# Optimization experiments

Measured on AMD Instinct MI355X. Metric: run time of the kernel, lower is better.

The kernel has to match this reference:

```python
import jax, jax.numpy as jnp
import numpy as np

N_CELLS, D_IN, D_HID, D_OUT, MLP_W = 16384, 512, 1024, 512, 128
N_FACTIONS, SYNC, DEBATE = 8, 0.15, 0.15


def setup_inputs() -> dict:
    key = jax.random.key(0)
    ks = jax.random.split(key, 20)
    s = 0.05
    inp = {
        "x": jax.random.normal(ks[0], (1, D_IN), jnp.float32),
        "hiddens": jax.random.normal(ks[1], (N_CELLS, D_HID), jnp.float32) * 0.1,
        "wealth_norm": jax.random.uniform(ks[2], (N_CELLS,), jnp.float32, 0.5, 1.5),
        "Wa1": jax.random.normal(ks[3], (D_IN + D_HID, MLP_W), jnp.float32) * s,
        "ba1": jax.random.normal(ks[4], (MLP_W,), jnp.float32) * s,
        "Wa2": jax.random.normal(ks[5], (MLP_W, D_OUT), jnp.float32) * s,
        "ba2": jax.random.normal(ks[6], (D_OUT,), jnp.float32) * s,
        "Wg1": jax.random.normal(ks[7], (D_IN + D_HID, MLP_W), jnp.float32) * s,
        "bg1": jax.random.normal(ks[8], (MLP_W,), jnp.float32) * s,
        "Wg2": jax.random.normal(ks[9], (MLP_W, D_OUT), jnp.float32) * s,
        "bg2": jax.random.normal(ks[10], (D_OUT,), jnp.float32) * s,
        "W_ih": jax.random.normal(ks[11], (D_OUT + 1, 3 * D_HID), jnp.float32) * s,
        "W_hh": jax.random.normal(ks[12], (D_HID, 3 * D_HID), jnp.float32) * s,
        "b_ih": jax.random.normal(ks[13], (3 * D_HID,), jnp.float32) * s,
        "b_hh": jax.random.normal(ks[14], (3 * D_HID,), jnp.float32) * s,
        "Wo": jax.random.normal(ks[15], (D_OUT, D_IN), jnp.float32) * s,
        "bo": jax.random.normal(ks[16], (D_IN,), jnp.float32) * s,
        "positions": jax.random.randint(ks[17], (N_CELLS,), 0, 3, jnp.int32) - 1,
        "step": 10,
    }
    return inp


def _gru_cell(mem, h, W_ih, W_hh, b_ih, b_hh):
    # torch.nn.GRUCell math, gate order r, z, n
    gi = mem @ W_ih + b_ih            # [N, 3H]
    gh = h @ W_hh + b_hh              # [N, 3H]
    gi_r, gi_z, gi_n = jnp.split(gi, 3, axis=-1)
    gh_r, gh_z, gh_n = jnp.split(gh, 3, axis=-1)
    r = jax.nn.sigmoid(gi_r + gh_r)
    z = jax.nn.sigmoid(gi_z + gh_z)
    n = jnp.tanh(gi_n + r * gh_n)
    return (1.0 - z) * n + z * h


def _group_sync(h, mask):
    cnt = jnp.sum(mask)
    m = mask[:, None].astype(h.dtype)
    mean = jnp.sum(h * m, axis=0) / jnp.maximum(cnt, 1).astype(h.dtype)
    blended = 0.9 * h + 0.1 * mean
    return jnp.where((mask[:, None]) & (cnt >= 2), blended, h)


def _faction_sync_debate(h, step):
    n = h.shape[0]
    n_f = min(N_FACTIONS, n // 2)
    if n_f < 2:
        return h
    fs = n // n_f
    hf = h[: n_f * fs].reshape(n_f, fs, -1)
    fmean = hf.mean(axis=1, keepdims=True)                    # [n_f, 1, H]
    hf = (1.0 - SYNC) * hf + SYNC * fmean
    if step > 5:
        global_op = hf.mean(axis=1).mean(axis=0)              # [H]
        dc = max(1, fs // 4)
        head = (1.0 - DEBATE) * hf[:, :dc] + DEBATE * global_op
        hf = jnp.concatenate([head, hf[:, dc:]], axis=1)
    out = hf.reshape(n_f * fs, -1)
    if n_f * fs < n:
        out = jnp.concatenate([out, h[n_f * fs:]], axis=0)
    return out


def reference(x, hiddens, wealth_norm, Wa1, ba1, Wa2, ba2, Wg1, bg1, Wg2, bg2,
              W_ih, W_hh, b_ih, b_hh, Wo, bo, positions, step):
    n = hiddens.shape[0]
    xb = jnp.broadcast_to(x, (n, x.shape[-1]))                # same x for every cell
    combined = jnp.concatenate([xb, hiddens], axis=-1)        # [N, D_in+D_hid]
    a = jax.nn.relu(combined @ Wa1 + ba1) @ Wa2 + ba2
    g = jax.nn.relu(combined @ Wg1 + bg1) @ Wg2 + bg2
    output = a - g                                            # [N, D_out]
    tension = jnp.mean(output ** 2, axis=-1, keepdims=True)   # [N, 1]
    mem_input = jax.lax.stop_gradient(jnp.concatenate([output, tension], axis=-1))
    new_h = _gru_cell(mem_input, hiddens, W_ih, W_hh, b_ih, b_hh)
    mod = 0.9 + 0.1 * jnp.clip(wealth_norm, 0.1, 2.0)
    new_h = jnp.clip(new_h * mod[:, None], -10.0, 10.0)
    new_h = jax.lax.stop_gradient(new_h)                      # original detaches state
    new_h = _group_sync(new_h, positions > 0)
    new_h = _group_sync(new_h, positions < 0)
    new_h = _faction_sync_debate(new_h, step)
    # tension weights come from .item() in torch -> constants
    weights = jax.nn.softmax(jax.lax.stop_gradient(tension[:, 0]))
    combined_out = weights @ output                           # [D_out]
    pred = (combined_out @ Wo + bo)[None, :]                  # [1, D_in]
    avg_tension = jnp.mean(tension)
    return pred, avg_tension, new_h
```

## Files before the change

kernel.cpp:

```cpp
#include <hip/hip_runtime.h>
#include <stdint.h>

typedef unsigned short u16;
typedef __bf16 bf16x8 __attribute__((ext_vector_type(8)));
typedef float f32x4 __attribute__((ext_vector_type(4)));


__device__ __forceinline__ float bf2f(unsigned u) { return __uint_as_float(u << 16); }
__device__ __forceinline__ u16 f2bf(float f) {
  unsigned x = __float_as_uint(f);
  unsigned r = x + 0x7fffu + ((x >> 16) & 1u);
  return (u16)(r >> 16);
}
__device__ __forceinline__ unsigned pack2(float a, float b) {
  return (unsigned)f2bf(a) | ((unsigned)f2bf(b) << 16);
}
__device__ __forceinline__ float sigm(float x) { return 1.f / (1.f + __expf(-x)); }
__device__ __forceinline__ float fast_tanh(float x) {
  float e = __expf(2.f * x);
  return 1.f - 2.f / (e + 1.f);
}

#define AS1(p) ((const __attribute__((address_space(1))) void*)(p))
#define AS3(p) ((__attribute__((address_space(3))) void*)(p))

#define NC 16384

__device__ __forceinline__ void packT_body(
    const float* __restrict__ src, int sld, int srow0,
    u16* __restrict__ dst, int dld, int drow0, int koff,
    int remapThresh, int remapAdd, float sgn, int bx, int by,
    float (*tile)[65], int t) {
  const int k0 = by * 64, c0 = bx * 64;
  const int tx = t & 15, ty = t >> 4;
#pragma unroll
  for (int p = 0; p < 4; ++p) {
    int r = ty + p * 16;
    float4 v = *reinterpret_cast<const float4*>(&src[(size_t)(srow0 + k0 + r) * sld + c0 + tx * 4]);
    tile[tx * 4 + 0][r] = v.x;
    tile[tx * 4 + 1][r] = v.y;
    tile[tx * 4 + 2][r] = v.z;
    tile[tx * 4 + 3][r] = v.w;
  }
  __syncthreads();
  const int cl = t >> 2;
  const int kb = (t & 3) * 16;
  int col = c0 + cl;
  int row = drow0 + col + ((col >= remapThresh) ? remapAdd : 0);
  union { u16 o[16]; uint4 v[2]; } u;
#pragma unroll
  for (int e = 0; e < 16; ++e) u.o[e] = f2bf(sgn * tile[cl][kb + e]);
  uint4* d = reinterpret_cast<uint4*>(&dst[(size_t)row * dld + koff + k0 + kb]);
  d[0] = u.v[0]; d[1] = u.v[1];
}

__global__ __launch_bounds__(256) void prep_kernel(
    const float* __restrict__ hid, u16* __restrict__ hidc,
    const float* __restrict__ W_ih, const float* __restrict__ W_hh, u16* __restrict__ WgruT,
    const float* __restrict__ Wa1, const float* __restrict__ Wg1, u16* __restrict__ W1catT,
    const float* __restrict__ Wa2, const float* __restrict__ Wg2, u16* __restrict__ W2catT,
    const float* __restrict__ x, const float* __restrict__ ba1, const float* __restrict__ bg1,
    float* __restrict__ bias1, const float* __restrict__ ba2, const float* __restrict__ bg2,
    float* __restrict__ bias2, const int* __restrict__ positions, int* __restrict__ counts) {
  __shared__ float tile[64][65];
  int b = blockIdx.x, t = threadIdx.x;
  if (b < 16384) {
    int i = b * 256 + t;
    float4 v = ((const float4*)hid)[i];
    uint2 o; o.x = pack2(v.x, v.y); o.y = pack2(v.z, v.w);
    ((uint2*)hidc)[i] = o;
    return;
  }
  b -= 16384;
  if (b < 768) {
    packT_body(W_hh, 3072, 0, WgruT, 1536, 0, 512, 2048, 1024, 1.f, b % 48, b / 48, tile, t);
    return;
  }
  b -= 768;
  if (b < 384) {
    packT_body(W_ih, 3072, 0, WgruT, 1536, 0, 0, 1 << 30, 0, 1.f, b % 48, b / 48, tile, t);
    return;
  }
  b -= 384;
  if (b < 32) { packT_body(Wa1, 128, 512, W1catT, 1024, 0, 0, 1 << 30, 0, 1.f, b % 2, b / 2, tile, t); return; }
  b -= 32;
  if (b < 32) { packT_body(Wg1, 128, 512, W1catT, 1024, 128, 0, 1 << 30, 0, 1.f, b % 2, b / 2, tile, t); return; }
  b -= 32;
  if (b < 16) { packT_body(Wa2, 512, 0, W2catT, 256, 0, 0, 1 << 30, 0, 1.f, b % 8, b / 8, tile, t); return; }
  b -= 16;
  if (b < 16) { packT_body(Wg2, 512, 0, W2catT, 256, 0, 128, 1 << 30, 0, -1.f, b % 8, b / 8, tile, t); return; }
  b -= 16;
  if (b < 8) {
    const float* W = (t < 128) ? Wa1 : Wg1;
    int cc = t & 127;
    float acc = 0.f;
    int k0 = b * 64;
    for (int k = k0; k < k0 + 64; ++k) acc += x[k] * W[(size_t)k * 128 + cc];
    if (b == 0) acc += (t < 128) ? ba1[cc] : bg1[cc];
    atomicAdd(&bias1[t], acc);
    return;
  }
  b -= 8;
  if (b < 2) { int n = b * 256 + t; bias2[n] = ba2[n] - bg2[n]; return; }
  b -= 2;
  {
    int i = b * 256 + t;
    int p = positions[i], f = i >> 11;
    if (p > 0) atomicAdd(&counts[f * 2], 1);
    else if (p < 0) atomicAdd(&counts[f * 2 + 1], 1);
  }
}

__global__ __launch_bounds__(256) void gemm_bt(
    const u16* __restrict__ A, int lda,
    const u16* __restrict__ Bt, int ldb,
    u16* __restrict__ C, int ldc,
    const float* __restrict__ bias, int epi, int K,
    float* __restrict__ tension) {
  __shared__ __align__(16) u16 As[128 * 32];
  __shared__ __align__(16) u16 Bs[128 * 32];
  const int tid = threadIdx.x;
  const int m0 = blockIdx.x * 128;
  const int n0 = blockIdx.y * 128;
  f32x4 acc[4][4] = {};
  const int lane = tid & 63;
  const int w = tid >> 6;
  const int mw = (w & 1) * 64, nw = (w >> 1) * 64;
  const int fr = lane & 15;
  const int q = lane >> 4;
  const int ar0 = tid >> 2;
  const int ag = ((tid & 3) ^ ((ar0 >> 1) & 3)) * 8;

  for (int kk = 0; kk < K; kk += 32) {
    __syncthreads();
    __builtin_amdgcn_global_load_lds(AS1(A + (size_t)(m0 + ar0) * lda + kk + ag), AS3(&As[tid * 8]), 16, 0, 0);
    __builtin_amdgcn_global_load_lds(AS1(A + (size_t)(m0 + ar0 + 64) * lda + kk + ag), AS3(&As[(tid + 256) * 8]), 16, 0, 0);
    __builtin_amdgcn_global_load_lds(AS1(Bt + (size_t)(n0 + ar0) * ldb + kk + ag), AS3(&Bs[tid * 8]), 16, 0, 0);
    __builtin_amdgcn_global_load_lds(AS1(Bt + (size_t)(n0 + ar0 + 64) * ldb + kk + ag), AS3(&Bs[(tid + 256) * 8]), 16, 0, 0);
    __syncthreads();
    bf16x8 af[4], bfv[4];
#pragma unroll
    for (int mt = 0; mt < 4; ++mt) {
      int r = mw + mt * 16 + fr;
      af[mt] = *reinterpret_cast<const bf16x8*>(&As[r * 32 + ((q ^ ((r >> 1) & 3)) * 8)]);
    }
#pragma unroll
    for (int nt = 0; nt < 4; ++nt) {
      int r = nw + nt * 16 + fr;
      bfv[nt] = *reinterpret_cast<const bf16x8*>(&Bs[r * 32 + ((q ^ ((r >> 1) & 3)) * 8)]);
    }
#pragma unroll
    for (int mt = 0; mt < 4; ++mt)
#pragma unroll
      for (int nt = 0; nt < 4; ++nt)
        acc[mt][nt] = __builtin_amdgcn_mfma_f32_16x16x32_bf16(af[mt], bfv[nt], acc[mt][nt], 0, 0, 0);
  }
  const int rq = q * 4;
#pragma unroll
  for (int mt = 0; mt < 4; ++mt) {
    float srow[4] = {0.f, 0.f, 0.f, 0.f};
#pragma unroll
    for (int nt = 0; nt < 4; ++nt) {
      int col = n0 + nw + nt * 16 + fr;
      f32x4 v = acc[mt][nt];
#pragma unroll
      for (int r = 0; r < 4; ++r) {
        int row = m0 + mw + mt * 16 + rq + r;
        float val = v[r] + bias[col];
        if (epi == 1) val = val > 0.f ? val : 0.f;
        else srow[r] += val * val;
        C[(size_t)row * ldc + col] = f2bf(val);
      }
    }
    if (epi == 3) {
#pragma unroll
      for (int r = 0; r < 4; ++r) {
        float s = srow[r];
        s += __shfl_xor(s, 1, 16); s += __shfl_xor(s, 2, 16);
        s += __shfl_xor(s, 4, 16); s += __shfl_xor(s, 8, 16);
        if (fr == 0) atomicAdd(&tension[m0 + mw + mt * 16 + rq + r], s);
      }
    }
  }
}

__global__ __launch_bounds__(512, 4) void gemm_gru(
    const u16* __restrict__ outbf, const u16* __restrict__ hidc,
    const u16* __restrict__ WgruT,
    const float* __restrict__ W_ihf, const float* __restrict__ bihf,
    const float* __restrict__ bhhf, const float* __restrict__ wealthf,
    const float* __restrict__ tension, u16* __restrict__ hpre) {
  __shared__ __align__(16) u16 As[128 * 32];
  __shared__ __align__(16) u16 Bs[3][64 * 32];
  const int tid = threadIdx.x;
  const int m0 = blockIdx.x * 128;
  const int j0 = blockIdx.y * 64;
  f32x4 acc[4][2][2] = {};
  const int lane = tid & 63;
  const int w = tid >> 6;
  const int mw = (w & 3) * 32, nw = (w >> 2) * 32;
  const int fr = lane & 15;
  const int q = lane >> 4;
  const int arow = tid >> 2;
  const int ag = ((tid & 3) ^ ((arow >> 1) & 3)) * 8;
  const int ct = tid & 255;
  const int brow = ct >> 2;
  const int bg = ((ct & 3) ^ ((brow >> 1) & 3)) * 8;
  const int bsel = tid >> 8;

#pragma unroll
  for (int phase = 0; phase < 2; ++phase) {
    const u16* Ap = phase ? hidc : outbf;
    const int lda = phase ? 1024 : 512;
    const int kbeg = phase ? 512 : 0;
    const int kend = phase ? 1536 : 512;
    const int growG = phase ? 3072 : 2048;
#pragma unroll 1
    for (int kk = kbeg; kk < kend; kk += 32) {
      const int ka = kk - kbeg;
      __syncthreads();
      __builtin_amdgcn_global_load_lds(AS1(Ap + (size_t)(m0 + arow) * lda + ka + ag), AS3(&As[tid * 8]), 16, 0, 0);
      if (bsel == 0) {
        __builtin_amdgcn_global_load_lds(AS1(WgruT + (size_t)(j0 + brow) * 1536 + kk + bg), AS3(&Bs[0][ct * 8]), 16, 0, 0);
        __builtin_amdgcn_global_load_lds(AS1(WgruT + (size_t)(growG + j0 + brow) * 1536 + kk + bg), AS3(&Bs[2][ct * 8]), 16, 0, 0);
      } else {
        __builtin_amdgcn_global_load_lds(AS1(WgruT + (size_t)(1024 + j0 + brow) * 1536 + kk + bg), AS3(&Bs[1][ct * 8]), 16, 0, 0);
      }
      __syncthreads();
      bf16x8 af[2], b0[2], b1[2], b2[2];
#pragma unroll
      for (int mt = 0; mt < 2; ++mt) {
        int r = mw + mt * 16 + fr;
        af[mt] = *reinterpret_cast<const bf16x8*>(&As[r * 32 + ((q ^ ((r >> 1) & 3)) * 8)]);
      }
#pragma unroll
      for (int nt = 0; nt < 2; ++nt) {
        int r = nw + nt * 16 + fr;
        int s = (q ^ ((r >> 1) & 3)) * 8;
        b0[nt] = *reinterpret_cast<const bf16x8*>(&Bs[0][r * 32 + s]);
        b1[nt] = *reinterpret_cast<const bf16x8*>(&Bs[1][r * 32 + s]);
        b2[nt] = *reinterpret_cast<const bf16x8*>(&Bs[2][r * 32 + s]);
      }
#pragma unroll
      for (int mt = 0; mt < 2; ++mt)
#pragma unroll
        for (int nt = 0; nt < 2; ++nt) {
          acc[0][mt][nt] = __builtin_amdgcn_mfma_f32_16x16x32_bf16(af[mt], b0[nt], acc[0][mt][nt], 0, 0, 0);
          acc[1][mt][nt] = __builtin_amdgcn_mfma_f32_16x16x32_bf16(af[mt], b1[nt], acc[1][mt][nt], 0, 0, 0);
          if (phase == 0)
            acc[2][mt][nt] = __builtin_amdgcn_mfma_f32_16x16x32_bf16(af[mt], b2[nt], acc[2][mt][nt], 0, 0, 0);
          else
            acc[3][mt][nt] = __builtin_amdgcn_mfma_f32_16x16x32_bf16(af[mt], b2[nt], acc[3][mt][nt], 0, 0, 0);
        }
    }
  }

  const int rq = q * 4;
  const float* wt = W_ihf + (size_t)512 * 3072;
  float wtr[2], wtz[2], wtn[2], bir[2], biz[2], bin_[2], bhr_[2], bhz_[2], bhn_[2];
#pragma unroll
  for (int nt = 0; nt < 2; ++nt) {
    int j = j0 + nw + nt * 16 + fr;
    wtr[nt] = wt[j]; wtz[nt] = wt[1024 + j]; wtn[nt] = wt[2048 + j];
    bir[nt] = bihf[j]; biz[nt] = bihf[1024 + j]; bin_[nt] = bihf[2048 + j];
    bhr_[nt] = bhhf[j]; bhz_[nt] = bhhf[1024 + j]; bhn_[nt] = bhhf[2048 + j];
  }
#pragma unroll
  for (int mt = 0; mt < 2; ++mt) {
#pragma unroll
    for (int rr = 0; rr < 4; ++rr) {
      int row = m0 + mw + mt * 16 + rq + rr;
      float tv = tension[row] * (1.f / 512.f);
      float wl = fminf(fmaxf(wealthf[row], 0.1f), 2.0f);
      float mod = 0.9f + 0.1f * wl;
#pragma unroll
      for (int nt = 0; nt < 2; ++nt) {
        int j = j0 + nw + nt * 16 + fr;
        float r = sigm(acc[0][mt][nt][rr] + tv * wtr[nt] + bir[nt] + bhr_[nt]);
        float z = sigm(acc[1][mt][nt][rr] + tv * wtz[nt] + biz[nt] + bhz_[nt]);
        float n = fast_tanh(acc[2][mt][nt][rr] + tv * wtn[nt] + bin_[nt]
                            + r * (acc[3][mt][nt][rr] + bhn_[nt]));
        float h = bf2f(hidc[(size_t)row * 1024 + j]);
        float h2 = (1.f - z) * n + z * h;
        h2 = fminf(fmaxf(h2 * mod, -10.f), 10.f);
        hpre[(size_t)row * 1024 + j] = f2bf(h2);
      }
    }
  }
}

__global__ void stats_kernel(const u16* __restrict__ hpre, const int* __restrict__ positions,
                             float* __restrict__ fsums) {
  int cc = blockIdx.x, f = blockIdx.y, z = blockIdx.z, t = threadIdx.x;
  int col = cc * 128 + (t & 127);
  int half = t >> 7;
  float st = 0, sp = 0, sm = 0;
  for (int it = 0; it < 128; ++it) {
    int row = (f << 11) + ((z * 128 + it) << 1) + half;
    int p = positions[row];
    float v = bf2f(hpre[(size_t)row * 1024 + col]);
    st += v;
    if (p > 0) sp += v;
    if (p < 0) sm += v;
  }
  atomicAdd(&fsums[(f * 3 + 0) * 1024 + col], st);
  atomicAdd(&fsums[(f * 3 + 1) * 1024 + col], sp);
  atomicAdd(&fsums[(f * 3 + 2) * 1024 + col], sm);
}

__global__ void derive_kernel(const float* __restrict__ fsums, const int* __restrict__ counts,
                              float* __restrict__ mean1, float* __restrict__ mean2,
                              float* __restrict__ fmean, float* __restrict__ gop,
                              float* __restrict__ scal) {
  int c = threadIdx.x;
  int cnt1 = 0, cnt2 = 0, cf1[8], cf2[8];
#pragma unroll
  for (int f = 0; f < 8; ++f) {
    cf1[f] = counts[f * 2]; cf2[f] = counts[f * 2 + 1];
    cnt1 += cf1[f]; cnt2 += cf2[f];
  }
  float s1 = 0, s2 = 0;
#pragma unroll
  for (int f = 0; f < 8; ++f) { s1 += fsums[(f * 3 + 1) * 1024 + c]; s2 += fsums[(f * 3 + 2) * 1024 + c]; }
  float m1 = s1 / (float)(cnt1 > 1 ? cnt1 : 1);
  float m2 = s2 / (float)(cnt2 > 1 ? cnt2 : 1);
  float a1 = (cnt1 >= 2) ? 0.1f : 0.f;
  float a2 = (cnt2 >= 2) ? 0.1f : 0.f;
  float g = 0;
#pragma unroll
  for (int f = 0; f < 8; ++f) {
    float fm = (fsums[(f * 3) * 1024 + c]
                + a1 * ((float)cf1[f] * m1 - fsums[(f * 3 + 1) * 1024 + c])
                + a2 * ((float)cf2[f] * m2 - fsums[(f * 3 + 2) * 1024 + c])) * (1.f / 2048.f);
    fmean[f * 1024 + c] = fm;
    g += fm;
  }
  gop[c] = g * 0.125f;
  mean1[c] = m1; mean2[c] = m2;
  if (c == 0) { scal[0] = a1; scal[1] = a2; }
}

__global__ void finalize_kernel(const u16* __restrict__ hpre, const int* __restrict__ positions,
                                const int* __restrict__ step, const float* __restrict__ mean1,
                                const float* __restrict__ mean2, const float* __restrict__ fmean,
                                const float* __restrict__ gop, const float* __restrict__ scal,
                                float* __restrict__ out) {
  int row = blockIdx.x, t = threadIdx.x;
  int p = positions[row];
  float w1 = (p > 0) ? scal[0] : 0.f;
  float w2 = (p < 0) ? scal[1] : 0.f;
  int f = row >> 11, q = row & 2047;
  bool deb = (step[0] > 5) && (q < 512);
  const u16* hrow = hpre + (size_t)row * 1024;
  const float* fmp = fmean + f * 1024;
  float* orow = out + 513 + (size_t)row * 1024;
#pragma unroll
  for (int e = 0; e < 8; ++e) {
    int c = e * 128 + t;
    float h = bf2f(hrow[c]);
    float hgs = h + w1 * (mean1[c] - h) + w2 * (mean2[c] - h);
    float hfs = 0.85f * hgs + 0.15f * fmp[c];
    orow[c] = deb ? (0.85f * hfs + 0.15f * gop[c]) : hfs;
  }
}

__global__ void softmax_kernel(const float* __restrict__ tension, float* __restrict__ weights,
                               float* __restrict__ out) {
  __shared__ float red[1024];
  int t = threadIdx.x;
  float tv[16], mx = -1e30f, sumt = 0.f;
#pragma unroll
  for (int k = 0; k < 16; ++k) {
    tv[k] = tension[t + k * 1024] * (1.f / 512.f);
    mx = fmaxf(mx, tv[k]); sumt += tv[k];
  }
  red[t] = mx; __syncthreads();
  for (int s = 512; s > 0; s >>= 1) { if (t < s) red[t] = fmaxf(red[t], red[t + s]); __syncthreads(); }
  float m = red[0]; __syncthreads();
  red[t] = sumt; __syncthreads();
  for (int s = 512; s > 0; s >>= 1) { if (t < s) red[t] += red[t + s]; __syncthreads(); }
  float tot = red[0]; __syncthreads();
  float ev[16], se = 0.f;
#pragma unroll
  for (int k = 0; k < 16; ++k) { ev[k] = __expf(tv[k] - m); se += ev[k]; }
  red[t] = se; __syncthreads();
  for (int s = 512; s > 0; s >>= 1) { if (t < s) red[t] += red[t + s]; __syncthreads(); }
  float invS = 1.f / red[0];
#pragma unroll
  for (int k = 0; k < 16; ++k) weights[t + k * 1024] = ev[k] * invS;
  if (t == 0) out[512] = tot * (1.f / 16384.f);
}

__global__ void wsum_kernel(const float* __restrict__ weights, const u16* __restrict__ outbf,
                            float* __restrict__ co) {
  int b = blockIdx.x, t = threadIdx.x;
  int c = t * 2;
  float a0 = 0.f, a1 = 0.f;
  int i0 = b * 128;
  for (int i = i0; i < i0 + 128; ++i) {
    float w = weights[i];
    unsigned v = *reinterpret_cast<const unsigned*>(outbf + (size_t)i * 512 + c);
    a0 += w * bf2f(v & 0xffff);
    a1 += w * bf2f(v >> 16);
  }
  atomicAdd(&co[c], a0);
  atomicAdd(&co[c + 1], a1);
}

__global__ void pred_kernel(const float* __restrict__ co, const float* __restrict__ Wof,
                            const float* __restrict__ bof, float* __restrict__ out) {
  __shared__ float cs[512];
  int t = threadIdx.x, n = blockIdx.x * 256 + t;
  cs[t] = co[t]; cs[t + 256] = co[t + 256];
  __syncthreads();
  float acc = bof[n];
  for (int ck = 0; ck < 512; ++ck) acc += cs[ck] * Wof[(size_t)ck * 512 + n];
  out[n] = acc;
}

extern "C" void kernel_launch(void* const* d_in, const int* in_sizes, int n_in,
                              void* d_out, int out_size, void* d_ws, size_t ws_size,
                              hipStream_t stream) {
  const float* x      = (const float*)d_in[0];
  const float* hid    = (const float*)d_in[1];
  const float* wealth = (const float*)d_in[2];
  const float* Wa1    = (const float*)d_in[3];
  const float* ba1    = (const float*)d_in[4];
  const float* Wa2    = (const float*)d_in[5];
  const float* ba2    = (const float*)d_in[6];
  const float* Wg1    = (const float*)d_in[7];
  const float* bg1    = (const float*)d_in[8];
  const float* Wg2    = (const float*)d_in[9];
  const float* bg2    = (const float*)d_in[10];
  const float* W_ih   = (const float*)d_in[11];
  const float* W_hh   = (const float*)d_in[12];
  const float* b_ih   = (const float*)d_in[13];
  const float* b_hh   = (const float*)d_in[14];
  const float* Wo     = (const float*)d_in[15];
  const float* bo     = (const float*)d_in[16];
  const int* positions= (const int*)d_in[17];
  const int* step     = (const int*)d_in[18];
  float* out = (float*)d_out;

  char* w = (char*)d_ws;
  size_t off = 0;
  auto alloc = [&](size_t bytes) { void* p = w + off; off += (bytes + 255) & ~(size_t)255; return p; };
  u16*   hidc    = (u16*)  alloc((size_t)NC * 1024 * 2);
  u16*   outbf   = (u16*)  alloc((size_t)NC * 512 * 2);
  u16*   hpre    = (u16*)  alloc((size_t)NC * 1024 * 2);
  u16*   WgruT   = (u16*)  alloc((size_t)4096 * 1536 * 2);
  u16*   W1catT  = (u16*)  alloc((size_t)256 * 1024 * 2);
  u16*   W2catT  = (u16*)  alloc((size_t)512 * 256 * 2);
  u16*   t1      = (u16*)  alloc((size_t)NC * 256 * 2);
  float* bias1   = (float*)alloc(256 * 4);
  float* co      = (float*)alloc(512 * 4);
  int*   counts  = (int*)  alloc(16 * 4);
  float* fsums   = (float*)alloc(8 * 3 * 1024 * 4);
  float* tension = (float*)alloc(NC * 4);
  float* bias2   = (float*)alloc(512 * 4);
  float* weights = (float*)alloc(NC * 4);
  float* mean1   = (float*)alloc(1024 * 4);
  float* mean2   = (float*)alloc(1024 * 4);
  float* gop     = (float*)alloc(1024 * 4);
  float* fmean   = (float*)alloc(8 * 1024 * 4);
  float* scal    = (float*)alloc(8 * 4);

  hipMemsetAsync(bias1, 0, 1024 + 2048 + 256 + 98304 + 65536, stream);

  prep_kernel<<<17706, 256, 0, stream>>>(hid, hidc, W_ih, W_hh, WgruT,
                                         Wa1, Wg1, W1catT, Wa2, Wg2, W2catT,
                                         x, ba1, bg1, bias1, ba2, bg2, bias2,
                                         positions, counts);

  gemm_bt<<<dim3(128, 2), 256, 0, stream>>>(hidc, 1024, W1catT, 1024, t1, 256,
                                            bias1, 1, 1024, nullptr);
  gemm_bt<<<dim3(128, 4), 256, 0, stream>>>(t1, 256, W2catT, 256, outbf, 512,
                                            bias2, 3, 256, tension);

  gemm_gru<<<dim3(128, 16), 512, 0, stream>>>(outbf, hidc, WgruT, W_ih, b_ih, b_hh,
                                              wealth, tension, hpre);

  stats_kernel<<<dim3(8, 8, 8), 256, 0, stream>>>(hpre, positions, fsums);
  derive_kernel<<<1, 1024, 0, stream>>>(fsums, counts, mean1, mean2, fmean, gop, scal);
  finalize_kernel<<<NC, 128, 0, stream>>>(hpre, positions, step, mean1, mean2, fmean, gop,
                                          scal, out);

  softmax_kernel<<<1, 1024, 0, stream>>>(tension, weights, out);
  wsum_kernel<<<128, 256, 0, stream>>>(weights, outbf, co);
  pred_kernel<<<2, 256, 0, stream>>>(co, Wo, bo, out);

  (void)in_sizes; (void)n_in; (void)out_size; (void)ws_size;
}
```

Baseline: 602.7 us.

## Triple-buffer LDS tiles with async prefetch in GEMM and GRU kernels

Both the generic bf16 GEMM and the fused GRU GEMM now keep three LDS stages and issue global_load_lds prefetches two k-steps ahead. Explicit vmcnt waits replace the two __syncthreads per iteration, and the MFMA block runs under raised wave priority. This is meant to hide global-memory latency behind the matrix math. The cost is triple the LDS footprint, which may reduce occupancy (especially for gemm_gru with 512-thread blocks and launch bounds 4). The hand-counted waitcnt values also add correctness risk.

```diff
diff --git a/kernel.cpp b/kernel.cpp
--- a/kernel.cpp
+++ b/kernel.cpp
@@ -117,8 +117,8 @@
     u16* __restrict__ C, int ldc,
     const float* __restrict__ bias, int epi, int K,
     float* __restrict__ tension) {
-  __shared__ __align__(16) u16 As[128 * 32];
-  __shared__ __align__(16) u16 Bs[128 * 32];
+  __shared__ __align__(16) u16 As[3][128 * 32];
+  __shared__ __align__(16) u16 Bs[3][128 * 32];
   const int tid = threadIdx.x;
   const int m0 = blockIdx.x * 128;
   const int n0 = blockIdx.y * 128;
@@ -131,29 +131,52 @@
   const int ar0 = tid >> 2;
   const int ag = ((tid & 3) ^ ((ar0 >> 1) & 3)) * 8;
 
-  for (int kk = 0; kk < K; kk += 32) {
-    __syncthreads();
-    __builtin_amdgcn_global_load_lds(AS1(A + (size_t)(m0 + ar0) * lda + kk + ag), AS3(&As[tid * 8]), 16, 0, 0);
-    __builtin_amdgcn_global_load_lds(AS1(A + (size_t)(m0 + ar0 + 64) * lda + kk + ag), AS3(&As[(tid + 256) * 8]), 16, 0, 0);
-    __builtin_amdgcn_global_load_lds(AS1(Bt + (size_t)(n0 + ar0) * ldb + kk + ag), AS3(&Bs[tid * 8]), 16, 0, 0);
-    __builtin_amdgcn_global_load_lds(AS1(Bt + (size_t)(n0 + ar0 + 64) * ldb + kk + ag), AS3(&Bs[(tid + 256) * 8]), 16, 0, 0);
-    __syncthreads();
+  const u16* aB0 = A + (size_t)(m0 + ar0) * lda + ag;
+  const u16* aB1 = A + (size_t)(m0 + ar0 + 64) * lda + ag;
+  const u16* bB0 = Bt + (size_t)(n0 + ar0) * ldb + ag;
+  const u16* bB1 = Bt + (size_t)(n0 + ar0 + 64) * ldb + ag;
+
+  auto stage = [&](int kk, int buf) {
+    __builtin_amdgcn_global_load_lds(AS1(aB0 + kk), AS3(&As[buf][tid * 8]), 16, 0, 0);
+    __builtin_amdgcn_global_load_lds(AS1(aB1 + kk), AS3(&As[buf][(tid + 256) * 8]), 16, 0, 0);
+    __builtin_amdgcn_global_load_lds(AS1(bB0 + kk), AS3(&Bs[buf][tid * 8]), 16, 0, 0);
+    __builtin_amdgcn_global_load_lds(AS1(bB1 + kk), AS3(&Bs[buf][(tid + 256) * 8]), 16, 0, 0);
+  };
+
+  const int NT = K >> 5;
+  stage(0, 0);
+  stage(32, 1);
+  int cur = 0, nxt = 1, nx2 = 2;
+#pragma unroll 1
+  for (int t = 0; t < NT; ++t) {
+    if (t + 2 < NT) stage((t + 2) * 32, nx2);
+    const int rem = NT - 1 - t;
+    if (rem >= 2)      asm volatile("s_waitcnt vmcnt(8)" ::: "memory");
+    else if (rem == 1) asm volatile("s_waitcnt vmcnt(4)" ::: "memory");
+    else               asm volatile("s_waitcnt vmcnt(0)" ::: "memory");
+    __builtin_amdgcn_s_barrier();
+    asm volatile("" ::: "memory");
     bf16x8 af[4], bfv[4];
 #pragma unroll
     for (int mt = 0; mt < 4; ++mt) {
       int r = mw + mt * 16 + fr;
-      af[mt] = *reinterpret_cast<const bf16x8*>(&As[r * 32 + ((q ^ ((r >> 1) & 3)) * 8)]);
+      af[mt] = *reinterpret_cast<const bf16x8*>(&As[cur][r * 32 + ((q ^ ((r >> 1) & 3)) * 8)]);
     }
 #pragma unroll
     for (int nt = 0; nt < 4; ++nt) {
       int r = nw + nt * 16 + fr;
-      bfv[nt] = *reinterpret_cast<const bf16x8*>(&Bs[r * 32 + ((q ^ ((r >> 1) & 3)) * 8)]);
+      bfv[nt] = *reinterpret_cast<const bf16x8*>(&Bs[cur][r * 32 + ((q ^ ((r >> 1) & 3)) * 8)]);
     }
+    __builtin_amdgcn_s_setprio(1);
 #pragma unroll
     for (int mt = 0; mt < 4; ++mt)
 #pragma unroll
       for (int nt = 0; nt < 4; ++nt)
         acc[mt][nt] = __builtin_amdgcn_mfma_f32_16x16x32_bf16(af[mt], bfv[nt], acc[mt][nt], 0, 0, 0);
+    __builtin_amdgcn_s_setprio(0);
+    asm volatile("s_waitcnt lgkmcnt(0)" ::: "memory");
+    __builtin_amdgcn_s_barrier();
+    int tmp = cur; cur = nxt; nxt = nx2; nx2 = tmp;
   }
   const int rq = q * 4;
 #pragma unroll
@@ -190,8 +213,8 @@
     const float* __restrict__ W_ihf, const float* __restrict__ bihf,
     const float* __restrict__ bhhf, const float* __restrict__ wealthf,
     const float* __restrict__ tension, u16* __restrict__ hpre) {
-  __shared__ __align__(16) u16 As[128 * 32];
-  __shared__ __align__(16) u16 Bs[3][64 * 32];
+  __shared__ __align__(16) u16 As[3][128 * 32];
+  __shared__ __align__(16) u16 Bs[3][3][64 * 32];
   const int tid = threadIdx.x;
   const int m0 = blockIdx.x * 128;
   const int j0 = blockIdx.y * 64;
@@ -208,52 +231,77 @@
   const int bg = ((ct & 3) ^ ((brow >> 1) & 3)) * 8;
   const int bsel = tid >> 8;
 
-#pragma unroll
-  for (int phase = 0; phase < 2; ++phase) {
-    const u16* Ap = phase ? hidc : outbf;
-    const int lda = phase ? 1024 : 512;
-    const int kbeg = phase ? 512 : 0;
-    const int kend = phase ? 1536 : 512;
-    const int growG = phase ? 3072 : 2048;
+  const u16* aB0 = outbf + (size_t)(m0 + arow) * 512 + ag;
+  const u16* aB1 = hidc + (size_t)(m0 + arow) * 1024 + ag;
+  const u16* bBR = WgruT + (size_t)((bsel ? 1024 : 0) + j0 + brow) * 1536 + bg;
+
+  auto stage = [&](int s, int buf) {
+    const int p = s >= 16;
+    const u16* ap = p ? (aB1 + (s - 16) * 32) : (aB0 + s * 32);
+    __builtin_amdgcn_global_load_lds(AS1(ap), AS3(&As[buf][tid * 8]), 16, 0, 0);
+    const int kk = s * 32;
+    if (bsel == 0) {
+      __builtin_amdgcn_global_load_lds(AS1(bBR + kk), AS3(&Bs[buf][0][ct * 8]), 16, 0, 0);
+      __builtin_amdgcn_global_load_lds(
+          AS1(bBR + (size_t)(2048 * 1536 + (p ? 1024 * 1536 : 0) + kk)),
+          AS3(&Bs[buf][2][ct * 8]), 16, 0, 0);
+    } else {
+      __builtin_amdgcn_global_load_lds(AS1(bBR + kk), AS3(&Bs[buf][1][ct * 8]), 16, 0, 0);
+    }
+  };
+
+  stage(0, 0);
+  stage(1, 1);
+  int cur = 0, nxt = 1, nx2 = 2;
+
+#define GRU_STEP(T, REG3)                                                                     \
+  {                                                                                           \
+    if ((T) < 46) {                                                                           \
+      stage((T) + 2, nx2);                                                                    \
+      if (bsel == 0) asm volatile("s_waitcnt vmcnt(6)" ::: "memory");                         \
+      else           asm volatile("s_waitcnt vmcnt(4)" ::: "memory");                         \
+    } else if ((T) == 46) {                                                                   \
+      if (bsel == 0) asm volatile("s_waitcnt vmcnt(3)" ::: "memory");                         \
+      else           asm volatile("s_waitcnt vmcnt(2)" ::: "memory");                         \
+    } else {                                                                                  \
+      asm volatile("s_waitcnt vmcnt(0)" ::: "memory");                                        \
+    }                                                                                         \
+    __builtin_amdgcn_s_barrier();                                                             \
+    asm volatile("" ::: "memory");                                                            \
+    bf16x8 af[2], b0v[2], b1v[2], b2v[2];                                                     \
+    _Pragma("unroll")                                                                         \
+    for (int mt = 0; mt < 2; ++mt) {                                                          \
+      int r = mw + mt * 16 + fr;                                                              \
+      af[mt] = *reinterpret_cast<const bf16x8*>(&As[cur][r * 32 + ((q ^ ((r >> 1) & 3)) * 8)]);\
+    }                                                                                         \
+    _Pragma("unroll")                                                                         \
+    for (int nt = 0; nt < 2; ++nt) {                                                          \
+      int r = nw + nt * 16 + fr;                                                              \
+      int ss = (q ^ ((r >> 1) & 3)) * 8;                                                      \
+      b0v[nt] = *reinterpret_cast<const bf16x8*>(&Bs[cur][0][r * 32 + ss]);                   \
+      b1v[nt] = *reinterpret_cast<const bf16x8*>(&Bs[cur][1][r * 32 + ss]);                   \
+      b2v[nt] = *reinterpret_cast<const bf16x8*>(&Bs[cur][2][r * 32 + ss]);                   \
+    }                                                                                         \
+    __builtin_amdgcn_s_setprio(1);                                                            \
+    _Pragma("unroll")                                                                         \
+    for (int mt = 0; mt < 2; ++mt)                                                            \
+      _Pragma("unroll")                                                                       \
+      for (int nt = 0; nt < 2; ++nt) {                                                        \
+        acc[0][mt][nt] = __builtin_amdgcn_mfma_f32_16x16x32_bf16(af[mt], b0v[nt], acc[0][mt][nt], 0, 0, 0); \
+        acc[1][mt][nt] = __builtin_amdgcn_mfma_f32_16x16x32_bf16(af[mt], b1v[nt], acc[1][mt][nt], 0, 0, 0); \
+        acc[REG3][mt][nt] = __builtin_amdgcn_mfma_f32_16x16x32_bf16(af[mt], b2v[nt], acc[REG3][mt][nt], 0, 0, 0); \
+      }                                                                                       \
+    __builtin_amdgcn_s_setprio(0);                                                            \
+    asm volatile("s_waitcnt lgkmcnt(0)" ::: "memory");                                        \
+    __builtin_amdgcn_s_barrier();                                                             \
+    int tmp = cur; cur = nxt; nxt = nx2; nx2 = tmp;                                           \
+  }
+
 #pragma unroll 1
-    for (int kk = kbeg; kk < kend; kk += 32) {
-      const int ka = kk - kbeg;
-      __syncthreads();
-      __builtin_amdgcn_global_load_lds(AS1(Ap + (size_t)(m0 + arow) * lda + ka + ag), AS3(&As[tid * 8]), 16, 0, 0);
-      if (bsel == 0) {
-        __builtin_amdgcn_global_load_lds(AS1(WgruT + (size_t)(j0 + brow) * 1536 + kk + bg), AS3(&Bs[0][ct * 8]), 16, 0, 0);
-        __builtin_amdgcn_global_load_lds(AS1(WgruT + (size_t)(growG + j0 + brow) * 1536 + kk + bg), AS3(&Bs[2][ct * 8]), 16, 0, 0);
-      } else {
-        __builtin_amdgcn_global_load_lds(AS1(WgruT + (size_t)(1024 + j0 + brow) * 1536 + kk + bg), AS3(&Bs[1][ct * 8]), 16, 0, 0);
-      }
-      __syncthreads();
-      bf16x8 af[2], b0[2], b1[2], b2[2];
-#pragma unroll
-      for (int mt = 0; mt < 2; ++mt) {
-        int r = mw + mt * 16 + fr;
-        af[mt] = *reinterpret_cast<const bf16x8*>(&As[r * 32 + ((q ^ ((r >> 1) & 3)) * 8)]);
-      }
-#pragma unroll
-      for (int nt = 0; nt < 2; ++nt) {
-        int r = nw + nt * 16 + fr;
-        int s = (q ^ ((r >> 1) & 3)) * 8;
-        b0[nt] = *reinterpret_cast<const bf16x8*>(&Bs[0][r * 32 + s]);
-        b1[nt] = *reinterpret_cast<const bf16x8*>(&Bs[1][r * 32 + s]);
-        b2[nt] = *reinterpret_cast<const bf16x8*>(&Bs[2][r * 32 + s]);
-      }
-#pragma unroll
-      for (int mt = 0; mt < 2; ++mt)
-#pragma unroll
-        for (int nt = 0; nt < 2; ++nt) {
-          acc[0][mt][nt] = __builtin_amdgcn_mfma_f32_16x16x32_bf16(af[mt], b0[nt], acc[0][mt][nt], 0, 0, 0);
-          acc[1][mt][nt] = __builtin_amdgcn_mfma_f32_16x16x32_bf16(af[mt], b1[nt], acc[1][mt][nt], 0, 0, 0);
-          if (phase == 0)
-            acc[2][mt][nt] = __builtin_amdgcn_mfma_f32_16x16x32_bf16(af[mt], b2[nt], acc[2][mt][nt], 0, 0, 0);
-          else
-            acc[3][mt][nt] = __builtin_amdgcn_mfma_f32_16x16x32_bf16(af[mt], b2[nt], acc[3][mt][nt], 0, 0, 0);
-        }
-    }
-  }
+  for (int t = 0; t < 16; ++t) GRU_STEP(t, 2)
+#pragma unroll 1
+  for (int t = 16; t < 48; ++t) GRU_STEP(t, 3)
+#undef GRU_STEP
 
   const int rq = q * 4;
   const float* wt = W_ihf + (size_t)512 * 3072;
```

After: 598.8 us. No clear change (-0.6%).
